# Optimization experiments

Measured on AMD Instinct MI355X. Metric: run time of the kernel, lower is better.

The kernel has to match this reference:

```python
import math
import jax, jax.numpy as jnp
import numpy as np

EMBED_DIM = 2048
NUM_HEADS = 16
DEPTH = 12
LAMBDA_INIT = 0.8 - 0.6 * math.exp(-0.3 * DEPTH)
LN_EPS = 1e-5


def setup_inputs() -> dict:
    key = jax.random.key(0)
    ks = jax.random.split(key, 9)
    D = EMBED_DIM
    hd = D // NUM_HEADS // 2  # 64
    B, T = 1, 2048
    w_std = D ** -0.5
    return {
        "x": jax.random.normal(ks[0], (B, T, D), jnp.float32),
        "Wq": jax.random.normal(ks[1], (D, D), jnp.float32) * w_std,
        "Wk": jax.random.normal(ks[2], (D, D), jnp.float32) * w_std,
        "Wv": jax.random.normal(ks[3], (D, D), jnp.float32) * w_std,
        "Wo": jax.random.normal(ks[4], (D, D), jnp.float32) * w_std,
        "lambda_q1": jax.random.normal(ks[5], (hd,), jnp.float32) * 0.1,
        "lambda_k1": jax.random.normal(ks[6], (hd,), jnp.float32) * 0.1,
        "lambda_q2": jax.random.normal(ks[7], (hd,), jnp.float32) * 0.1,
        "lambda_k2": jax.random.normal(ks[8], (hd,), jnp.float32) * 0.1,
    }


def reference(x, Wq, Wk, Wv, Wo, lambda_q1, lambda_k1, lambda_q2, lambda_k2):
    B, T, D = x.shape
    hd = lambda_q1.shape[0]
    H = D // (2 * hd)  # num_heads
    scale = hd ** -0.5

    # projections (torch Linear, no bias); n_rep == 1 so k/v are full width
    q = (x @ Wq).reshape(B, T, 2 * H, hd).transpose(0, 2, 1, 3) * scale  # (B,2H,T,hd)
    k = (x @ Wk).reshape(B, T, 2 * H, hd).transpose(0, 2, 1, 3)          # (B,2H,T,hd)
    v = (x @ Wv).reshape(B, T, H, 2 * hd).transpose(0, 2, 1, 3)          # (B,H,T,2hd)

    # dual-stream attention logits with causal mask (offset = 0)
    attn = jnp.einsum("bhqd,bhkd->bhqk", q, k)  # (B,2H,T,T)
    mask = jnp.triu(jnp.full((T, T), -jnp.inf, dtype=attn.dtype), 1)
    attn = jax.nn.softmax((attn + mask).astype(jnp.float32), axis=-1).astype(x.dtype)

    # lambda reparameterization
    lam1 = jnp.exp(jnp.sum(lambda_q1 * lambda_k1))
    lam2 = jnp.exp(jnp.sum(lambda_q2 * lambda_k2))
    lam = lam1 - lam2 + LAMBDA_INIT

    attn = attn.reshape(B, H, 2, T, T)
    diff = attn[:, :, 0] - lam * attn[:, :, 1]  # (B,H,T,T)
    out = jnp.einsum("bhqk,bhkd->bhqd", diff, v)  # (B,H,T,2hd)

    # subln: LayerNorm over last dim (2hd), no affine, biased variance
    mu = jnp.mean(out, axis=-1, keepdims=True)
    var = jnp.mean(jnp.square(out - mu), axis=-1, keepdims=True)
    out = (out - mu) / jnp.sqrt(var + LN_EPS)
    out = out * (1.0 - LAMBDA_INIT)

    # NOTE: faithful to original -- reshape WITHOUT transposing heads back
    out = out.reshape(B, T, H * 2 * hd)
    return out @ Wo
```

## Files before the change

kernel.cpp:

```cpp
#include <hip/hip_runtime.h>
#include <hip/hip_bf16.h>


typedef unsigned short u16;
typedef __attribute__((ext_vector_type(4))) float f32x4;
typedef __attribute__((ext_vector_type(8))) short bf16x8;

#define LAMBDA_INIT  0.7836057665317954f
#define ONE_MINUS_LI 0.2163942334682046f
#define QSCALE 0.18033688011112042f

#define EXP2F(x) __builtin_amdgcn_exp2f(x)

__device__ __forceinline__ u16 f2bf(float f) {
    union { float f; unsigned u; } v; v.f = f;
    unsigned r = v.u + 0x7FFFu + ((v.u >> 16) & 1u);
    return (u16)(r >> 16);
}

__device__ __forceinline__ unsigned pkbf(float a, float b) {
    union { __hip_bfloat162 h; unsigned u; } c;
    c.h = __float22bfloat162_rn(make_float2(a, b));
    return c.u;
}

__device__ __forceinline__ void gld_lds16(const u16* g, u16* l) {
    __builtin_amdgcn_global_load_lds((const __attribute__((address_space(1))) void*)g,
                                     (__attribute__((address_space(3))) void*)l, 16, 0, 0);
}

__global__ void prep_inputs(const float* __restrict__ x, const float* __restrict__ W0,
                            const float* __restrict__ W1, const float* __restrict__ W2,
                            const float* __restrict__ W3,
                            u16* __restrict__ xb, u16* __restrict__ O0, u16* __restrict__ O1,
                            u16* __restrict__ O2, u16* __restrict__ O3) {
    __shared__ float tile[64][65];
    const int z = blockIdx.z;
    const int c0 = blockIdx.x * 64, r0 = blockIdx.y * 64;
    const int t = threadIdx.x;
    const int lr = t >> 2, lc = (t & 3) << 4;

    if (z == 4) {
        const float* src = x + (size_t)(r0 + lr) * 2048 + c0 + lc;
        uint ou[8];
#pragma unroll
        for (int jj = 0; jj < 4; jj++) {
            float4 v = *(const float4*)(src + 4 * jj);
            ou[2 * jj + 0] = pkbf(v.x, v.y);
            ou[2 * jj + 1] = pkbf(v.z, v.w);
        }
        u16* dst = xb + (size_t)(r0 + lr) * 2048 + c0 + lc;
        *(uint4*)(dst) = *(uint4*)&ou[0];
        *(uint4*)(dst + 8) = *(uint4*)&ou[4];
        return;
    }

    const float* W = z == 0 ? W0 : z == 1 ? W1 : z == 2 ? W2 : W3;
    u16* Wt = z == 0 ? O0 : z == 1 ? O1 : z == 2 ? O2 : O3;
#pragma unroll
    for (int jj = 0; jj < 4; jj++) {
        float4 v = *(const float4*)(W + (size_t)(r0 + lr) * 2048 + c0 + lc + 4 * jj);
        tile[lr][lc + 4 * jj + 0] = v.x;
        tile[lr][lc + 4 * jj + 1] = v.y;
        tile[lr][lc + 4 * jj + 2] = v.z;
        tile[lr][lc + 4 * jj + 3] = v.w;
    }
    __syncthreads();
    const int oc = t >> 2, op = (t & 3) << 4;
    uint ou[8];
#pragma unroll
    for (int k = 0; k < 8; k++)
        ou[k] = pkbf(tile[op + 2 * k][oc], tile[op + 2 * k + 1][oc]);
    u16* dst = Wt + (size_t)(c0 + oc) * 2048 + r0 + op;
    *(uint4*)(dst) = *(uint4*)&ou[0];
    *(uint4*)(dst + 8) = *(uint4*)&ou[4];
}

__device__ __forceinline__ void gemm_core_q(const u16* __restrict__ A, const u16* __restrict__ B,
                                            u16* __restrict__ Cout, float scale, int m0, int n0) {
    __shared__ __align__(16) u16 As[2][128 * 32];
    __shared__ __align__(16) u16 Bs[2][128 * 32];
    const int tid = threadIdx.x;
    const int lane = tid & 63, w = tid >> 6;
    const int wr = w >> 1, wc = w & 1;
    const int q16 = lane & 15, g = lane >> 4;
    const f32x4 fzero = {0.f, 0.f, 0.f, 0.f};
    f32x4 acc[4][4];
#pragma unroll
    for (int m = 0; m < 4; m++)
#pragma unroll
        for (int n = 0; n < 4; n++) acc[m][n] = fzero;

#define STGQ(buf, kb)                                                                \
    {                                                                                \
        _Pragma("unroll") for (int p = 0; p < 2; p++) {                              \
            int s = p * 256 + tid;                \
            int row = s >> 2, gc = s & 3;                                            \
            int sg = (gc ^ (row >> 1)) & 3;                                          \
            gld_lds16(A + (size_t)(m0 + row) * 2048 + (kb) + sg * 8, As[buf] + s * 8); \
            gld_lds16(B + (size_t)(n0 + row) * 2048 + (kb) + sg * 8, Bs[buf] + s * 8); \
        }                                                                            \
    }

    STGQ(0, 0);
    int cur = 0;
    for (int kb = 0; kb < 2048; kb += 32) {
        if (kb + 32 < 2048) {
            STGQ(cur ^ 1, kb + 32);
            asm volatile("s_waitcnt vmcnt(4)" ::: "memory");
        } else {
            asm volatile("s_waitcnt vmcnt(0)" ::: "memory");
        }
        __builtin_amdgcn_s_barrier();
        bf16x8 af[4], bfr[4];
#pragma unroll
        for (int m = 0; m < 4; m++) {
            const int R = wr * 64 + m * 16 + q16;
            af[m] = *(const bf16x8*)(As[cur] + R * 32 + 8 * ((g ^ (R >> 1)) & 3));
        }
#pragma unroll
        for (int n = 0; n < 4; n++) {
            const int R = wc * 64 + n * 16 + q16;
            bfr[n] = *(const bf16x8*)(Bs[cur] + R * 32 + 8 * ((g ^ (R >> 1)) & 3));
        }
        __builtin_amdgcn_s_setprio(1);
#pragma unroll
        for (int m = 0; m < 4; m++)
#pragma unroll
            for (int n = 0; n < 4; n++)
                acc[m][n] = __builtin_amdgcn_mfma_f32_16x16x32_bf16(af[m], bfr[n], acc[m][n], 0, 0, 0);
        __builtin_amdgcn_s_setprio(0);
        asm volatile("s_waitcnt lgkmcnt(0)" ::: "memory");
        __builtin_amdgcn_s_barrier();
        cur ^= 1;
    }
#pragma unroll
    for (int m = 0; m < 4; m++)
#pragma unroll
        for (int n = 0; n < 4; n++) {
            int row = m0 + wr * 64 + m * 16 + 4 * g;
            int col = n0 + wc * 64 + n * 16 + q16;
#pragma unroll
            for (int r = 0; r < 4; r++)
                Cout[(size_t)(row + r) * 2048 + col] = f2bf(acc[m][n][r] * scale);
        }
#undef STGQ
}

__device__ __forceinline__ void gemm_core64(const u16* __restrict__ A, const u16* __restrict__ B,
                                            float* __restrict__ Cout, float scale, int m0, int n0) {
    __shared__ __align__(16) u16 As[2][128 * 64];
    __shared__ __align__(16) u16 Bs[2][64 * 64];
    const int tid = threadIdx.x;
    const int lane = tid & 63, w = tid >> 6;
    const int q16 = lane & 15, g = lane >> 4;
    const int sw = q16 & 7;
    const f32x4 fzero = {0.f, 0.f, 0.f, 0.f};
    f32x4 acc[2][4];
#pragma unroll
    for (int m = 0; m < 2; m++)
#pragma unroll
        for (int n = 0; n < 4; n++) acc[m][n] = fzero;

#define STG64(buf, kb)                                                               \
    {                                                                                \
        _Pragma("unroll") for (int p = 0; p < 4; p++) {                              \
            int s = p * 256 + tid;                             \
            int row = s >> 3, sg = (s ^ row) & 7;                                    \
            gld_lds16(A + (size_t)(m0 + row) * 2048 + (kb) + sg * 8, As[buf] + s * 8); \
        }                                                                            \
        _Pragma("unroll") for (int p = 0; p < 2; p++) {                              \
            int s = p * 256 + tid;                              \
            int row = s >> 3, sg = (s ^ row) & 7;                                    \
            gld_lds16(B + (size_t)(n0 + row) * 2048 + (kb) + sg * 8, Bs[buf] + s * 8); \
        }                                                                            \
    }

    STG64(0, 0);
    int cur = 0;
    for (int kb = 0; kb < 2048; kb += 64) {
        if (kb + 64 < 2048) {
            STG64(cur ^ 1, kb + 64);
            asm volatile("s_waitcnt vmcnt(6)" ::: "memory");
        } else {
            asm volatile("s_waitcnt vmcnt(0)" ::: "memory");
        }
        __builtin_amdgcn_s_barrier();
        bf16x8 af[2][2], bfr[4][2];
#pragma unroll
        for (int m = 0; m < 2; m++) {
            const u16* ar = As[cur] + (w * 32 + m * 16 + q16) * 64;
            af[m][0] = *(const bf16x8*)(ar + 8 * (g ^ sw));
            af[m][1] = *(const bf16x8*)(ar + 8 * ((4 + g) ^ sw));
        }
#pragma unroll
        for (int n = 0; n < 4; n++) {
            const u16* br = Bs[cur] + (n * 16 + q16) * 64;
            bfr[n][0] = *(const bf16x8*)(br + 8 * (g ^ sw));
            bfr[n][1] = *(const bf16x8*)(br + 8 * ((4 + g) ^ sw));
        }
        __builtin_amdgcn_s_setprio(1);
#pragma unroll
        for (int m = 0; m < 2; m++)
#pragma unroll
            for (int n = 0; n < 4; n++) {
                acc[m][n] = __builtin_amdgcn_mfma_f32_16x16x32_bf16(af[m][0], bfr[n][0], acc[m][n], 0, 0, 0);
                acc[m][n] = __builtin_amdgcn_mfma_f32_16x16x32_bf16(af[m][1], bfr[n][1], acc[m][n], 0, 0, 0);
            }
        __builtin_amdgcn_s_setprio(0);
        asm volatile("s_waitcnt lgkmcnt(0)" ::: "memory");
        __builtin_amdgcn_s_barrier();
        cur ^= 1;
    }
#pragma unroll
    for (int m = 0; m < 2; m++)
#pragma unroll
        for (int n = 0; n < 4; n++) {
            int row = m0 + w * 32 + m * 16 + 4 * g;
            int col = n0 + n * 16 + q16;
#pragma unroll
            for (int r = 0; r < 4; r++)
                Cout[(size_t)(row + r) * 2048 + col] = acc[m][n][r] * scale;
        }
#undef STG64
}

__global__ __launch_bounds__(256, 4) void gemm_qkv(const u16* __restrict__ xb,
                                                   const u16* __restrict__ Wqt, const u16* __restrict__ Wkt,
                                                   const u16* __restrict__ Wvt,
                                                   u16* __restrict__ Qb, u16* __restrict__ Kb,
                                                   u16* __restrict__ Vtb) {
    const int id = blockIdx.x;
    const int ord = (id & 7) * 96 + (id >> 3);
    const int which = ord >> 8, r = ord & 255;
    const int m0 = (r & 15) * 128, n0 = (r >> 4) * 128;
    const u16 *A, *B; u16* C; float sc;
    if (which == 0)      { A = xb;  B = Wqt; C = Qb;  sc = QSCALE; }
    else if (which == 1) { A = xb;  B = Wkt; C = Kb;  sc = 1.f; }
    else                 { A = Wvt; B = xb;  C = Vtb; sc = 1.f; }
    gemm_core_q(A, B, C, sc, m0, n0);
}

__global__ __launch_bounds__(256, 3) void gemm_out(const u16* __restrict__ Mb, const u16* __restrict__ Wot,
                                                   float* __restrict__ out) {
    const int id = blockIdx.x;
    const int ord = (id & 7) * 64 + (id >> 3);
    const int m0 = (ord & 15) * 128, n0 = (ord >> 4) * 64;
    gemm_core64(Mb, Wot, out, 1.f, m0, n0);
}

__global__ __launch_bounds__(256, 2) void diff_attn(const u16* __restrict__ Qg, const u16* __restrict__ Kg,
                                                    const u16* __restrict__ Vg, u16* __restrict__ Mg,
                                                    const float* __restrict__ lq1, const float* __restrict__ lk1,
                                                    const float* __restrict__ lq2, const float* __restrict__ lk2) {
    __shared__ __align__(16) u16 smem[40960];
    const int tid = threadIdx.x;
    const int lane = tid & 63, w = tid >> 6;
    const int q16 = lane & 15, g = lane >> 4;
    const int sw = q16 & 7;
    const int id = blockIdx.x;
    const int xcd = id & 7, jj = id >> 3;
    const int p = jj >> 1, o = jj & 1;
    const int A = (p < 16) ? (32 - p) : (p - 15);
    const int s = o ? (33 - A) : A;
    const int qi = s - 1;
    const int h = (xcd << 1) | o;
    const int q0 = qi * 64;
    const int qg = q0 + 16 * w + q16;

    u16* Kb0 = smem;
    u16* Vb0 = smem + 8192;
    u16* Kb1 = smem + 16384;
    u16* Vb1 = smem + 24576;
    u16* Pw = smem + 32768 + w * 2048;

    bf16x8 qf[2][2];
#pragma unroll
    for (int st = 0; st < 2; st++)
#pragma unroll
        for (int db = 0; db < 2; db++)
            qf[st][db] = *(const bf16x8*)(Qg + (size_t)qg * 2048 + 128 * h + 64 * st + 32 * db + 8 * g);

#define STAGE_K(dst, kb)                                                         \
    {                                                                            \
        _Pragma("unroll") for (int p2 = 0; p2 < 4; p2++) {                       \
            int s2 = p2 * 256 + tid;                                             \
            int row = s2 >> 4, gc = s2 & 15;                                     \
            int sg = (gc ^ row) & 15;                                            \
            gld_lds16(Kg + (size_t)((kb) + row) * 2048 + 128 * h + sg * 8, (dst) + s2 * 8); \
        }                                                                        \
    }
#define STAGE_V(dst, kb)                                                         \
    {                                                                            \
        _Pragma("unroll") for (int p2 = 0; p2 < 4; p2++) {                       \
            int s2 = p2 * 256 + tid;                                             \
            int row = s2 >> 3, sg = (s2 ^ row) & 7;                              \
            gld_lds16(Vg + (size_t)(128 * h + row) * 2048 + (kb) + sg * 8, (dst) + s2 * 8); \
        }                                                                        \
    }

    const f32x4 fzero = {0.f, 0.f, 0.f, 0.f};
    f32x4 Oacc[2][8];
#pragma unroll
    for (int st = 0; st < 2; st++)
#pragma unroll
        for (int dt = 0; dt < 8; dt++) Oacc[st][dt] = fzero;
    float den[2] = {0.f, 0.f};

    const int nt = qi + 1;
    STAGE_K(Kb0, 0);
    STAGE_V(Vb0, 0);
    int cur = 0;
    for (int t = 0; t < nt; t++) {
        const int kb = t * 64;
        const u16* Ks = cur ? Kb1 : Kb0;
        const u16* Vs = cur ? Vb1 : Vb0;
        if (t + 1 < nt) {
            STAGE_K(cur ? Kb0 : Kb1, kb + 64);
            STAGE_V(cur ? Vb0 : Vb1, kb + 64);
            asm volatile("s_waitcnt vmcnt(8)" ::: "memory");
        } else {
            asm volatile("s_waitcnt vmcnt(0)" ::: "memory");
        }
        __builtin_amdgcn_s_barrier();

        f32x4 sc[2][4];
        __builtin_amdgcn_s_setprio(1);
#pragma unroll
        for (int st = 0; st < 2; st++)
#pragma unroll
            for (int kt = 0; kt < 4; kt++) {
                const u16* kr = Ks + (kt * 16 + q16) * 128;
                bf16x8 kf0 = *(const bf16x8*)(kr + 8 * ((st * 8 + g) ^ q16));
                bf16x8 kf1 = *(const bf16x8*)(kr + 8 * ((st * 8 + 4 + g) ^ q16));
                f32x4 a = __builtin_amdgcn_mfma_f32_16x16x32_bf16(kf0, qf[st][0], fzero, 0, 0, 0);
                a = __builtin_amdgcn_mfma_f32_16x16x32_bf16(kf1, qf[st][1], a, 0, 0, 0);
                sc[st][kt] = a;
            }
        __builtin_amdgcn_s_setprio(0);

        const bool last = (t == nt - 1);
#pragma unroll
        for (int st = 0; st < 2; st++) {
            u16* Pst = Pw + st * 1024;
            float dl = 0.f;
#pragma unroll
            for (int kt = 0; kt < 4; kt++) {
                float p0 = EXP2F(sc[st][kt][0]);
                float p1 = EXP2F(sc[st][kt][1]);
                float p2 = EXP2F(sc[st][kt][2]);
                float p3 = EXP2F(sc[st][kt][3]);
                if (last) {
                    const int kgi = kb + kt * 16 + 4 * g;
                    p0 = (kgi + 0 <= qg) ? p0 : 0.f;
                    p1 = (kgi + 1 <= qg) ? p1 : 0.f;
                    p2 = (kgi + 2 <= qg) ? p2 : 0.f;
                    p3 = (kgi + 3 <= qg) ? p3 : 0.f;
                }
                dl += (p0 + p1) + (p2 + p3);
                uint2 pr;
                pr.x = pkbf(p0, p1);
                pr.y = pkbf(p2, p3);
                *(uint2*)(Pst + q16 * 64 + ((kt * 16 + 4 * g) ^ (8 * sw))) = pr;
            }
            den[st] += dl;
        }

        bf16x8 pf[2][2];
#pragma unroll
        for (int st = 0; st < 2; st++)
#pragma unroll
            for (int kh = 0; kh < 2; kh++)
                pf[st][kh] = *(const bf16x8*)(Pw + st * 1024 + q16 * 64 + ((kh * 32 + 8 * g) ^ (8 * sw)));
        __builtin_amdgcn_s_setprio(1);
#pragma unroll
        for (int kh = 0; kh < 2; kh++)
#pragma unroll
            for (int dt = 0; dt < 8; dt++) {
                bf16x8 vf = *(const bf16x8*)(Vs + (dt * 16 + q16) * 64 + 8 * ((kh * 4 + g) ^ sw));
                Oacc[0][dt] = __builtin_amdgcn_mfma_f32_16x16x32_bf16(vf, pf[0][kh], Oacc[0][dt], 0, 0, 0);
                Oacc[1][dt] = __builtin_amdgcn_mfma_f32_16x16x32_bf16(vf, pf[1][kh], Oacc[1][dt], 0, 0, 0);
            }
        __builtin_amdgcn_s_setprio(0);
        asm volatile("s_waitcnt lgkmcnt(0)" ::: "memory");
        __builtin_amdgcn_s_barrier();
        cur ^= 1;
    }
#undef STAGE_K
#undef STAGE_V

    float sl1 = 0.f, sl2 = 0.f;
    for (int i = 0; i < 64; i++) { sl1 += lq1[i] * lk1[i]; sl2 += lq2[i] * lk2[i]; }
    const float lam = expf(sl1) - expf(sl2) + LAMBDA_INIT;

    float d0 = den[0], d1 = den[1];
    d0 += __shfl_xor(d0, 16); d0 += __shfl_xor(d0, 32);
    d1 += __shfl_xor(d1, 16); d1 += __shfl_xor(d1, 32);
    const float i1 = 1.f / d0;
    const float i2 = lam / d1;
    float S1 = 0.f, S2 = 0.f;
#pragma unroll
    for (int dt = 0; dt < 8; dt++)
#pragma unroll
        for (int r = 0; r < 4; r++) {
            float v = Oacc[0][dt][r] * i1 - Oacc[1][dt][r] * i2;
            S1 += v; S2 += v * v;
        }
    S1 += __shfl_xor(S1, 16); S1 += __shfl_xor(S1, 32);
    S2 += __shfl_xor(S2, 16); S2 += __shfl_xor(S2, 32);
    const float mu = S1 * (1.f / 128.f);
    const float var = S2 * (1.f / 128.f) - mu * mu;
    const float rs = rsqrtf(var + 1e-5f) * ONE_MINUS_LI;

    const int R = h * 128 + (q0 >> 4) + w;
    u16* drow = Mg + (size_t)R * 2048 + q16 * 128;
#pragma unroll
    for (int dt = 0; dt < 8; dt++) {
        float v0 = (Oacc[0][dt][0] * i1 - Oacc[1][dt][0] * i2 - mu) * rs;
        float v1 = (Oacc[0][dt][1] * i1 - Oacc[1][dt][1] * i2 - mu) * rs;
        float v2 = (Oacc[0][dt][2] * i1 - Oacc[1][dt][2] * i2 - mu) * rs;
        float v3 = (Oacc[0][dt][3] * i1 - Oacc[1][dt][3] * i2 - mu) * rs;
        uint2 oo;
        oo.x = pkbf(v0, v1);
        oo.y = pkbf(v2, v3);
        *(uint2*)(drow + dt * 16 + 4 * g) = oo;
    }
}

extern "C" void kernel_launch(void* const* d_in, const int* in_sizes, int n_in,
                              void* d_out, int out_size, void* d_ws, size_t ws_size,
                              hipStream_t stream) {
    (void)in_sizes; (void)n_in; (void)out_size; (void)ws_size;
    const float* x = (const float*)d_in[0];
    const float* Wq = (const float*)d_in[1];
    const float* Wk = (const float*)d_in[2];
    const float* Wv = (const float*)d_in[3];
    const float* Wo = (const float*)d_in[4];
    const float* lq1 = (const float*)d_in[5];
    const float* lk1 = (const float*)d_in[6];
    const float* lq2 = (const float*)d_in[7];
    const float* lk2 = (const float*)d_in[8];

    u16* ws = (u16*)d_ws;
    const size_t SZ = 2048u * 2048u;
    u16* xb = ws;
    u16* Wqt = ws + SZ;
    u16* Wkt = ws + 2 * SZ;
    u16* Wvt = ws + 3 * SZ;
    u16* Wot = ws + 4 * SZ;
    u16* Qb = ws + 5 * SZ;
    u16* Kb = ws + 6 * SZ;
    u16* Vtb = ws + 7 * SZ;
    u16* Mb = ws + 8 * SZ;

    prep_inputs<<<dim3(32, 32, 5), 256, 0, stream>>>(x, Wq, Wk, Wv, Wo, xb, Wqt, Wkt, Wvt, Wot);

    gemm_qkv<<<768, 256, 0, stream>>>(xb, Wqt, Wkt, Wvt, Qb, Kb, Vtb);

    diff_attn<<<512, 256, 0, stream>>>(Qb, Kb, Vtb, Mb, lq1, lk1, lq2, lk2);

    gemm_out<<<512, 256, 0, stream>>>(Mb, Wot, (float*)d_out);
}
```

Measured before the change: 164.3 us.

## Enlarge QKV GEMM tiles to 256x256 with 8-wave blocks and split-K pipelining

Rewrites the fused QKV projection GEMM to use 256x256 output tiles per 512-thread block (8 waves, each computing 128x64), launching 192 blocks instead of 768. Each 64-wide K step is split into two 32-wide halves whose global-to-LDS loads are interleaved with the MFMA phases, with finer-grained vmcnt waits. The aim is more data reuse per loaded tile and better overlap of loads with compute. The trade-offs are fewer blocks than CUs, higher register pressure from 32 accumulators, and LDS reads without the previous XOR swizzle, which may cause bank conflicts.

```diff
diff --git a/kernel.cpp b/kernel.cpp
--- a/kernel.cpp
+++ b/kernel.cpp
@@ -76,75 +76,112 @@
     *(uint4*)(dst + 8) = *(uint4*)&ou[4];
 }
 
-__device__ __forceinline__ void gemm_core_q(const u16* __restrict__ A, const u16* __restrict__ B,
-                                            u16* __restrict__ Cout, float scale, int m0, int n0) {
-    __shared__ __align__(16) u16 As[2][128 * 32];
-    __shared__ __align__(16) u16 Bs[2][128 * 32];
+__global__ __launch_bounds__(512, 2) void gemm_qkv(const u16* __restrict__ xb,
+                                                   const u16* __restrict__ Wqt, const u16* __restrict__ Wkt,
+                                                   const u16* __restrict__ Wvt,
+                                                   u16* __restrict__ Qb, u16* __restrict__ Kb,
+                                                   u16* __restrict__ Vtb) {
+    __shared__ __align__(16) u16 lds[2][2][2][256 * 32];
     const int tid = threadIdx.x;
-    const int lane = tid & 63, w = tid >> 6;
-    const int wr = w >> 1, wc = w & 1;
+    const int lane = tid & 63, wv = tid >> 6;
+    const int wm = wv >> 2, wn = wv & 3;
     const int q16 = lane & 15, g = lane >> 4;
+
+    const int id = blockIdx.x;
+    const int ord = (id & 7) * 24 + (id >> 3);
+    const int which = ord / 64, r = ord % 64;
+    const int m0 = (r & 7) * 256, n0 = (r >> 3) * 256;
+    const u16 *Ap, *Bp; u16* Cp; float sc;
+    if (which == 0)      { Ap = xb;  Bp = Wqt; Cp = Qb;  sc = QSCALE; }
+    else if (which == 1) { Ap = xb;  Bp = Wkt; Cp = Kb;  sc = 1.f; }
+    else                 { Ap = Wvt; Bp = xb;  Cp = Vtb; sc = 1.f; }
+
+#define STAGE_HALF(buf, type, kk, kb)                                                  \
+    {                                                                                  \
+        const u16* _src = (type) == 0 ? Ap : Bp;                                       \
+        const int _b0 = (type) == 0 ? m0 : n0;                                         \
+        u16* _dst = &lds[buf][type][kk][0];                                            \
+        _Pragma("unroll") for (int _i = 0; _i < 2; _i++) {                             \
+            int _s = _i * 512 + tid;                                                   \
+            int _row = _s >> 2, _gr = _s & 3;                                          \
+            gld_lds16(_src + (size_t)(_b0 + _row) * 2048 + (kb) + (kk) * 32 + _gr * 8, \
+                      _dst + _s * 8);                                                  \
+        }                                                                              \
+    }
+
     const f32x4 fzero = {0.f, 0.f, 0.f, 0.f};
-    f32x4 acc[4][4];
-#pragma unroll
-    for (int m = 0; m < 4; m++)
+    f32x4 acc[8][4];
+#pragma unroll
+    for (int m = 0; m < 8; m++)
 #pragma unroll
         for (int n = 0; n < 4; n++) acc[m][n] = fzero;
 
-#define STGQ(buf, kb)                                                                \
-    {                                                                                \
-        _Pragma("unroll") for (int p = 0; p < 2; p++) {                              \
-            int s = p * 256 + tid;                \
-            int row = s >> 2, gc = s & 3;                                            \
-            int sg = (gc ^ (row >> 1)) & 3;                                          \
-            gld_lds16(A + (size_t)(m0 + row) * 2048 + (kb) + sg * 8, As[buf] + s * 8); \
-            gld_lds16(B + (size_t)(n0 + row) * 2048 + (kb) + sg * 8, Bs[buf] + s * 8); \
-        }                                                                            \
-    }
-
-    STGQ(0, 0);
-    int cur = 0;
-    for (int kb = 0; kb < 2048; kb += 32) {
-        if (kb + 32 < 2048) {
-            STGQ(cur ^ 1, kb + 32);
-            asm volatile("s_waitcnt vmcnt(4)" ::: "memory");
-        } else {
-            asm volatile("s_waitcnt vmcnt(0)" ::: "memory");
-        }
-        __builtin_amdgcn_s_barrier();
-        bf16x8 af[4], bfr[4];
-#pragma unroll
-        for (int m = 0; m < 4; m++) {
-            const int R = wr * 64 + m * 16 + q16;
-            af[m] = *(const bf16x8*)(As[cur] + R * 32 + 8 * ((g ^ (R >> 1)) & 3));
-        }
+    STAGE_HALF(0, 0, 0, 0);
+    STAGE_HALF(0, 1, 0, 0);
+    STAGE_HALF(0, 0, 1, 0);
+    STAGE_HALF(0, 1, 1, 0);
+    asm volatile("s_waitcnt vmcnt(4)" ::: "memory");
+    __builtin_amdgcn_s_barrier();
+
+    const int NT = 32;
+    for (int t = 0; t < NT; t++) {
+        const int buf = t & 1, nbuf = buf ^ 1;
+        const int kbn = (t + 1) * 64;
+        const bool more = (t + 1 < NT);
+        bf16x8 af[8];
+#pragma unroll
+        for (int p = 0; p < 4; p++) {
+            const int kk = p >> 1, nh = p & 1;
+            if (nh == 0) {
+#pragma unroll
+                for (int m = 0; m < 8; m++) {
+                    int row = wm * 128 + m * 16 + q16;
+                    af[m] = *(const bf16x8*)(&lds[buf][0][kk][row * 32 + 8 * g]);
+                }
+            }
+            bf16x8 bf0, bf1;
+            {
+                int rb0 = wn * 64 + (2 * nh + 0) * 16 + q16;
+                int rb1 = wn * 64 + (2 * nh + 1) * 16 + q16;
+                bf0 = *(const bf16x8*)(&lds[buf][1][kk][rb0 * 32 + 8 * g]);
+                bf1 = *(const bf16x8*)(&lds[buf][1][kk][rb1 * 32 + 8 * g]);
+            }
+            if (more) {
+                if (p == 0)      STAGE_HALF(nbuf, 0, 0, kbn)
+                else if (p == 1) STAGE_HALF(nbuf, 1, 0, kbn)
+                else if (p == 2) STAGE_HALF(nbuf, 0, 1, kbn)
+                else             STAGE_HALF(nbuf, 1, 1, kbn)
+            }
+            __builtin_amdgcn_s_barrier();
+            asm volatile("s_waitcnt lgkmcnt(0)" ::: "memory");
+            __builtin_amdgcn_s_setprio(1);
+#pragma unroll
+            for (int m = 0; m < 8; m++) {
+                acc[m][2 * nh + 0] = __builtin_amdgcn_mfma_f32_16x16x32_bf16(af[m], bf0, acc[m][2 * nh + 0], 0, 0, 0);
+                acc[m][2 * nh + 1] = __builtin_amdgcn_mfma_f32_16x16x32_bf16(af[m], bf1, acc[m][2 * nh + 1], 0, 0, 0);
+            }
+            __builtin_amdgcn_s_setprio(0);
+            if (p == 1) {
+                if (more) asm volatile("s_waitcnt vmcnt(4)" ::: "memory");
+                else      asm volatile("s_waitcnt vmcnt(0)" ::: "memory");
+            } else if (p == 3) {
+                asm volatile("s_waitcnt vmcnt(4)" ::: "memory");
+            }
+            __builtin_amdgcn_s_barrier();
+        }
+    }
+#undef STAGE_HALF
+
+#pragma unroll
+    for (int m = 0; m < 8; m++)
 #pragma unroll
         for (int n = 0; n < 4; n++) {
-            const int R = wc * 64 + n * 16 + q16;
-            bfr[n] = *(const bf16x8*)(Bs[cur] + R * 32 + 8 * ((g ^ (R >> 1)) & 3));
-        }
-        __builtin_amdgcn_s_setprio(1);
-#pragma unroll
-        for (int m = 0; m < 4; m++)
-#pragma unroll
-            for (int n = 0; n < 4; n++)
-                acc[m][n] = __builtin_amdgcn_mfma_f32_16x16x32_bf16(af[m], bfr[n], acc[m][n], 0, 0, 0);
-        __builtin_amdgcn_s_setprio(0);
-        asm volatile("s_waitcnt lgkmcnt(0)" ::: "memory");
-        __builtin_amdgcn_s_barrier();
-        cur ^= 1;
-    }
-#pragma unroll
-    for (int m = 0; m < 4; m++)
-#pragma unroll
-        for (int n = 0; n < 4; n++) {
-            int row = m0 + wr * 64 + m * 16 + 4 * g;
-            int col = n0 + wc * 64 + n * 16 + q16;
-#pragma unroll
-            for (int r = 0; r < 4; r++)
-                Cout[(size_t)(row + r) * 2048 + col] = f2bf(acc[m][n][r] * scale);
-        }
-#undef STGQ
+            int row = m0 + wm * 128 + m * 16 + 4 * g;
+            int col = n0 + wn * 64 + n * 16 + q16;
+#pragma unroll
+            for (int rr = 0; rr < 4; rr++)
+                Cp[(size_t)(row + rr) * 2048 + col] = f2bf(acc[m][n][rr] * sc);
+        }
 }
 
 __device__ __forceinline__ void gemm_core64(const u16* __restrict__ A, const u16* __restrict__ B,
@@ -223,22 +260,6 @@
                 Cout[(size_t)(row + r) * 2048 + col] = acc[m][n][r] * scale;
         }
 #undef STG64
-}
-
-__global__ __launch_bounds__(256, 4) void gemm_qkv(const u16* __restrict__ xb,
-                                                   const u16* __restrict__ Wqt, const u16* __restrict__ Wkt,
-                                                   const u16* __restrict__ Wvt,
-                                                   u16* __restrict__ Qb, u16* __restrict__ Kb,
-                                                   u16* __restrict__ Vtb) {
-    const int id = blockIdx.x;
-    const int ord = (id & 7) * 96 + (id >> 3);
-    const int which = ord >> 8, r = ord & 255;
-    const int m0 = (r & 15) * 128, n0 = (r >> 4) * 128;
-    const u16 *A, *B; u16* C; float sc;
-    if (which == 0)      { A = xb;  B = Wqt; C = Qb;  sc = QSCALE; }
-    else if (which == 1) { A = xb;  B = Wkt; C = Kb;  sc = 1.f; }
-    else                 { A = Wvt; B = xb;  C = Vtb; sc = 1.f; }
-    gemm_core_q(A, B, C, sc, m0, n0);
 }
 
 __global__ __launch_bounds__(256, 3) void gemm_out(const u16* __restrict__ Mb, const u16* __restrict__ Wot,
@@ -455,7 +476,7 @@
 
     prep_inputs<<<dim3(32, 32, 5), 256, 0, stream>>>(x, Wq, Wk, Wv, Wo, xb, Wqt, Wkt, Wvt, Wot);
 
-    gemm_qkv<<<768, 256, 0, stream>>>(xb, Wqt, Wkt, Wvt, Qb, Kb, Vtb);
+    gemm_qkv<<<192, 512, 0, stream>>>(xb, Wqt, Wkt, Wvt, Qb, Kb, Vtb);
 
     diff_attn<<<512, 256, 0, stream>>>(Qb, Kb, Vtb, Mb, lq1, lk1, lq2, lk2);
 
```

Result: slower. 168.5 us (+2.5%).
